# Kernel optimization log

Hardware: AMD Instinct MI355X
Metric: run time of the kernel (lower is better)

Reference implementation:

```python
import jax, jax.numpy as jnp
import numpy as np

N_E, E_DIM = 2048, 256
B, H, W = 32, 32, 32


def setup_inputs() -> dict:
    key = jax.random.key(0)
    k1, k2 = jax.random.split(key)
    z = jax.random.normal(k1, (B, E_DIM, H, W), dtype=jnp.float32)
    embedding = jax.random.normal(k2, (N_E, E_DIM), dtype=jnp.float32)
    return {"z": z, "embedding": embedding}


def reference(z, embedding):
    # z: [B, C, H, W] with C == e_dim; embedding: [n_e, e_dim]
    n_e, e_dim = embedding.shape
    b, c, h, w = z.shape
    z_nhwc = jnp.transpose(z, (0, 2, 3, 1))            # [B,H,W,C]
    z_flat = z_nhwc.reshape(-1, e_dim)                 # [L, D]
    # squared euclidean distance: ||z||^2 + ||e||^2 - 2 z.e^T
    d = (
        jnp.sum(z_flat * z_flat, axis=1, keepdims=True)
        + jnp.sum(embedding * embedding, axis=1)
        - 2.0 * jnp.einsum("ld,nd->ln", z_flat, embedding)
    )                                                  # [L, n_e]
    idx = jnp.argmin(d, axis=1)                        # [L]
    z_q = jnp.take(embedding, idx, axis=0).reshape(b, h, w, e_dim)
    # embed_ema=True -> commitment-only loss (codebook updated by EMA, not grads)
    loss = jnp.mean((jax.lax.stop_gradient(z_q) - z_nhwc) ** 2)
    # straight-through estimator
    z_q_st = z_nhwc + jax.lax.stop_gradient(z_q - z_nhwc)
    quantize = jnp.transpose(z_q_st, (0, 3, 1, 2))     # [B,C,H,W]
    # number of distinct codebook entries used (jit-safe via scatter-set)
    used = jnp.sum(jnp.zeros((n_e,), z.dtype).at[idx].set(1.0))
    index = idx.reshape(b, h, w)
    return quantize, loss, index, used
```

## Files before the change

kernel.cpp:

```cpp
#include <hip/hip_runtime.h>
#include <cfloat>

#define Dm 256
#define HW 1024
#define NE 2048
#define L_TOT 32768
#define QOFF 8388608
#define TAU 0.02f

typedef __attribute__((ext_vector_type(8))) short bf16x8;
typedef __attribute__((ext_vector_type(4))) float f32x4;
typedef const __attribute__((address_space(1))) unsigned int* as1_u32p;
typedef __attribute__((address_space(3))) unsigned int* as3_u32p;

#define GLL(gp, lp) __builtin_amdgcn_global_load_lds((as1_u32p)(gp), (as3_u32p)(lp), 16, 0, 0)

__device__ __forceinline__ unsigned short f2bf(float x) {
    unsigned u = __float_as_uint(x);
    unsigned r = (u + 0x7fffu + ((u >> 16) & 1u)) >> 16;
    return (unsigned short)r;
}
__device__ __forceinline__ float bf2f(unsigned short h) {
    return __uint_as_float(((unsigned)h) << 16);
}

__global__ void k_enorm(const float* __restrict__ emb, float* __restrict__ enorm) {
    int w = threadIdx.x >> 6, lane = threadIdx.x & 63;
    int n = blockIdx.x * 4 + w;
    const float4 v = *reinterpret_cast<const float4*>(emb + (size_t)n * Dm + lane * 4);
    double s = (double)v.x * v.x + (double)v.y * v.y + (double)v.z * v.z + (double)v.w * v.w;
    #pragma unroll
    for (int off = 32; off; off >>= 1) s += __shfl_xor(s, off);
    if (lane == 0) enorm[n] = (float)s;
}

__global__ __launch_bounds__(256) void k_split_e_norm(
    const float* __restrict__ emb, unsigned short* __restrict__ e_hi,
    unsigned short* __restrict__ e_lo, float* __restrict__ enorm)
{
    int w = threadIdx.x >> 6, lane = threadIdx.x & 63;
    int n = blockIdx.x * 4 + w;
    const float4 v = *reinterpret_cast<const float4*>(emb + (size_t)n * Dm + lane * 4);
    float vv[4] = { v.x, v.y, v.z, v.w };
    double s = (double)v.x * v.x + (double)v.y * v.y + (double)v.z * v.z + (double)v.w * v.w;
    #pragma unroll
    for (int off = 32; off; off >>= 1) s += __shfl_xor(s, off);
    if (lane == 0) enorm[n] = (float)s;
    ushort4 h4, l4;
    unsigned short* hp = (unsigned short*)&h4;
    unsigned short* lp = (unsigned short*)&l4;
    #pragma unroll
    for (int j = 0; j < 4; ++j) {
        unsigned short h = f2bf(vv[j]);
        hp[j] = h;
        lp[j] = f2bf(vv[j] - bf2f(h));
    }
    *reinterpret_cast<ushort4*>(e_hi + (size_t)n * Dm + lane * 4) = h4;
    *reinterpret_cast<ushort4*>(e_lo + (size_t)n * Dm + lane * 4) = l4;
}

__global__ __launch_bounds__(256) void k_split_z(const float* __restrict__ z,
                                                 unsigned short* __restrict__ z_hi,
                                                 unsigned short* __restrict__ z_lo,
                                                 float* __restrict__ zn_part) {
    __shared__ unsigned short zh[32][260];
    __shared__ unsigned short zl[32][260];
    __shared__ double zsum[4];
    const int b  = blockIdx.x >> 5;
    const int p0 = (blockIdx.x & 31) * 32;
    const int t  = threadIdx.x;
    const int pp = t & 31, cb = t >> 5;
    const float* zb = z + (size_t)b * (Dm * HW) + p0 + pp;
    float zs = 0.f;
    for (int ci = 0; ci < 32; ++ci) {
        int c = ci * 8 + cb;
        float x = zb[(size_t)c * HW];
        zs = fmaf(x, x, zs);
        unsigned short h = f2bf(x);
        zh[pp][c] = h;
        zl[pp][c] = f2bf(x - bf2f(h));
    }
    double d = zs;
    #pragma unroll
    for (int off = 32; off; off >>= 1) d += __shfl_xor(d, off);
    if ((t & 63) == 0) zsum[t >> 6] = d;
    __syncthreads();
    if (t == 0) zn_part[blockIdx.x] = (float)(zsum[0] + zsum[1] + zsum[2] + zsum[3]);
    const int l0 = b * 1024 + p0;
    #pragma unroll
    for (int r = 0; r < 8; ++r) {
        int id = r * 256 + t;
        int row = id >> 6, ch = id & 63;
        *reinterpret_cast<ushort4*>(z_hi + (size_t)(l0 + row) * Dm + ch * 4) =
            *reinterpret_cast<ushort4*>(&zh[row][ch * 4]);
        *reinterpret_cast<ushort4*>(z_lo + (size_t)(l0 + row) * Dm + ch * 4) =
            *reinterpret_cast<ushort4*>(&zl[row][ch * 4]);
    }
}

__global__ __launch_bounds__(512, 4) void k_score2(
    const unsigned short* __restrict__ z_hi, const unsigned short* __restrict__ z_lo,
    const unsigned short* __restrict__ e_hi, const unsigned short* __restrict__ e_lo,
    const float* __restrict__ enorm,
    float* __restrict__ pd1, float* __restrict__ pd2, int* __restrict__ pi1)
{
    __shared__ unsigned short lds[2][2][128 * 64];

    const int t    = threadIdx.x;
    const int lane = t & 63, w = t >> 6;
    const int wm = w >> 2, wn = w & 3;
    const int c15 = lane & 15, g4 = lane >> 4;

    const int bx = blockIdx.x;
    const int wg = (bx & 7) * 64 + (bx >> 3);
    const int mi = wg >> 1, ni = wg & 1;
    const int l0 = mi * 128;
    const int nbase = ni * 1024;

    auto stage = [&](int buf, const unsigned short* As, const unsigned short* Bs,
                     int nB0, int k0) {
        #pragma unroll
        for (int r = 0; r < 2; ++r) {
            int id  = r * 512 + t;
            int row = id >> 3, ch = id & 7;
            int chg = ch ^ (row & 7);
            GLL(As + (size_t)(l0 + row) * Dm + k0 + chg * 8, &lds[buf][0][id * 8]);
            GLL(Bs + (size_t)(nB0 + row) * Dm + k0 + chg * 8, &lds[buf][1][id * 8]);
        }
    };

    float d1[4][4], d2[4][4]; int i1[4][4];
    #pragma unroll
    for (int m = 0; m < 4; ++m)
        #pragma unroll
        for (int r = 0; r < 4; ++r) { d1[m][r] = 3.4e38f; d2[m][r] = 3.4e38f; i1[m][r] = 0; }

    stage(0, z_hi, e_hi, nbase, 0);
    __syncthreads();

    int cur = 0, it = 0;
    for (int nt = 0; nt < 8; ++nt) {
        f32x4 acc[4][2];
        #pragma unroll
        for (int m = 0; m < 4; ++m)
            #pragma unroll
            for (int n = 0; n < 2; ++n) acc[m][n] = (f32x4){0.f, 0.f, 0.f, 0.f};

        for (int kt = 0; kt < 12; ++kt, ++it) {
            if (it + 1 < 96) {
                int nit = it + 1;
                int nnt = nit / 12;
                int nkt = nit - nnt * 12;
                int nterm = nkt >> 2, nkc = nkt & 3;
                const unsigned short* As = (nterm == 1) ? z_lo : z_hi;
                const unsigned short* Bs = (nterm == 2) ? e_lo : e_hi;
                stage(cur ^ 1, As, Bs, nbase + nnt * 128, nkc * 64);
            }
            const unsigned short* Ab = &lds[cur][0][0];
            const unsigned short* Bb = &lds[cur][1][0];
            #pragma unroll
            for (int ks = 0; ks < 2; ++ks) {
                bf16x8 af[4], bfr[2];
                #pragma unroll
                for (int m = 0; m < 4; ++m) {
                    int row = wm * 64 + m * 16 + c15;
                    int cc  = ks * 4 + g4;
                    af[m] = *reinterpret_cast<const bf16x8*>(
                        &Ab[row * 64 + ((cc ^ (row & 7)) << 3)]);
                }
                #pragma unroll
                for (int n = 0; n < 2; ++n) {
                    int row = wn * 32 + n * 16 + c15;
                    int cc  = ks * 4 + g4;
                    bfr[n] = *reinterpret_cast<const bf16x8*>(
                        &Bb[row * 64 + ((cc ^ (row & 7)) << 3)]);
                }
                __builtin_amdgcn_s_setprio(1);
                #pragma unroll
                for (int m = 0; m < 4; ++m)
                    #pragma unroll
                    for (int n = 0; n < 2; ++n)
                        acc[m][n] = __builtin_amdgcn_mfma_f32_16x16x32_bf16(
                            af[m], bfr[n], acc[m][n], 0, 0, 0);
                __builtin_amdgcn_s_setprio(0);
            }
            __syncthreads();
            cur ^= 1;
        }
        int n0 = nbase + nt * 128;
        #pragma unroll
        for (int n = 0; n < 2; ++n) {
            int ng = n0 + wn * 32 + n * 16 + c15;
            float en = enorm[ng];
            #pragma unroll
            for (int m = 0; m < 4; ++m)
                #pragma unroll
                for (int r = 0; r < 4; ++r) {
                    float s = fmaf(-2.f, acc[m][n][r], en);
                    if (s < d1[m][r]) { d2[m][r] = d1[m][r]; d1[m][r] = s; i1[m][r] = ng; }
                    else if (s < d2[m][r]) d2[m][r] = s;
                }
        }
    }

    #pragma unroll
    for (int off = 1; off <= 8; off <<= 1) {
        #pragma unroll
        for (int m = 0; m < 4; ++m)
            #pragma unroll
            for (int r = 0; r < 4; ++r) {
                float od1 = __shfl_xor(d1[m][r], off);
                int   oi1 = __shfl_xor(i1[m][r], off);
                float od2 = __shfl_xor(d2[m][r], off);
                float nd2 = fminf(fminf(d2[m][r], od2), fmaxf(d1[m][r], od1));
                if (od1 < d1[m][r] || (od1 == d1[m][r] && oi1 < i1[m][r])) {
                    d1[m][r] = od1; i1[m][r] = oi1;
                }
                d2[m][r] = nd2;
            }
    }

    float* rs1 = (float*)&lds[0][0][0];
    float* rs2 = rs1 + 3 * 128;
    int*   ri  = (int*)(rs2 + 3 * 128);
    if (wn > 0 && c15 == 0) {
        int s = wn - 1;
        #pragma unroll
        for (int m = 0; m < 4; ++m)
            #pragma unroll
            for (int r = 0; r < 4; ++r) {
                int q = wm * 64 + m * 16 + g4 * 4 + r;
                rs1[s * 128 + q] = d1[m][r];
                rs2[s * 128 + q] = d2[m][r];
                ri [s * 128 + q] = i1[m][r];
            }
    }
    __syncthreads();
    if (wn == 0 && c15 == 0) {
        #pragma unroll
        for (int m = 0; m < 4; ++m)
            #pragma unroll
            for (int r = 0; r < 4; ++r) {
                int q = wm * 64 + m * 16 + g4 * 4 + r;
                float bd1 = d1[m][r], bd2 = d2[m][r]; int bi1 = i1[m][r];
                #pragma unroll
                for (int s = 0; s < 3; ++s) {
                    float od1 = rs1[s * 128 + q], od2 = rs2[s * 128 + q];
                    int   oi1 = ri [s * 128 + q];
                    float nd2 = fminf(fminf(bd2, od2), fmaxf(bd1, od1));
                    if (od1 < bd1 || (od1 == bd1 && oi1 < bi1)) { bd1 = od1; bi1 = oi1; }
                    bd2 = nd2;
                }
                int gq = l0 + q;
                pd1[ni * L_TOT + gq] = bd1;
                pd2[ni * L_TOT + gq] = bd2;
                pi1[ni * L_TOT + gq] = bi1;
            }
    }
}

__global__ __launch_bounds__(256) void k_merge(
    const float* __restrict__ pd1, const float* __restrict__ pd2,
    const int* __restrict__ pi1, int* __restrict__ ws_idx,
    float* __restrict__ out_idxf, float* __restrict__ used,
    int* __restrict__ flag_cnt, int* __restrict__ flag_list,
    float* __restrict__ d1_part)
{
    __shared__ float sdl[256];
    int tt = threadIdx.x;
    int gq = blockIdx.x * 256 + tt;
    float d1 = pd1[gq], d2 = pd2[gq]; int i1 = pi1[gq];
    {
        float od1 = pd1[L_TOT + gq], od2 = pd2[L_TOT + gq];
        int   oi1 = pi1[L_TOT + gq];
        float nd2 = fminf(fminf(d2, od2), fmaxf(d1, od1));
        if (od1 < d1 || (od1 == d1 && oi1 < i1)) { d1 = od1; i1 = oi1; }
        d2 = nd2;
    }
    ws_idx[gq] = i1;
    out_idxf[gq] = (float)i1;
    if (d2 - d1 < TAU) {
        int pos = atomicAdd(flag_cnt, 1);
        flag_list[pos] = gq;
    } else {
        used[i1] = 1.0f;
    }
    sdl[tt] = d1;
    __syncthreads();
    for (int st = 128; st; st >>= 1) {
        if (tt < st) sdl[tt] += sdl[tt + st];
        __syncthreads();
    }
    if (tt == 0) d1_part[blockIdx.x] = sdl[0];
}

#define BM 64
#define BN 128
#define BK 64
__global__ __launch_bounds__(256, 2) void k_argmin_f32(
    const float* __restrict__ z, const float* __restrict__ emb,
    const float* __restrict__ enorm, int* __restrict__ ws_idx,
    float* __restrict__ out_idxf, float* __restrict__ used,
    int* __restrict__ flag_cnt, int* __restrict__ flag_list)
{
    __shared__ float zl[BK][BM];
    __shared__ float el[BK][BN + 4];
    __shared__ float rd1[4][64];
    __shared__ int   ri1[4][64];
    __shared__ float rd2[4][64];

    const int t  = threadIdx.x;
    const int tq = t & 15;
    const int tn = t >> 4;
    const int l0 = blockIdx.x * BM;
    const int b  = l0 >> 10, p0 = l0 & 1023;
    const float* zb = z + (size_t)b * (Dm * HW) + p0;

    float d1[4], d2[4]; int i1[4];
    #pragma unroll
    for (int i = 0; i < 4; ++i) { d1[i] = FLT_MAX; d2[i] = FLT_MAX; i1[i] = 0; }

    for (int nt = 0; nt < NE / BN; ++nt) {
        const int n0 = nt * BN;
        float acc[4][8];
        #pragma unroll
        for (int i = 0; i < 4; ++i)
            #pragma unroll
            for (int j = 0; j < 8; ++j) acc[i][j] = 0.f;

        for (int kc = 0; kc < Dm / BK; ++kc) {
            __syncthreads();
            #pragma unroll
            for (int r = 0; r < 4; ++r) {
                int f = r * 256 + t;
                int kk = f >> 4, q4 = (f & 15) << 2;
                float4 v = *reinterpret_cast<const float4*>(zb + (size_t)(kc * BK + kk) * HW + q4);
                *reinterpret_cast<float4*>(&zl[kk][q4]) = v;
            }
            #pragma unroll
            for (int r = 0; r < 8; ++r) {
                int f = r * 256 + t;
                int n = f >> 4, k4 = (f & 15) << 2;
                float4 v = *reinterpret_cast<const float4*>(emb + (size_t)(n0 + n) * Dm + kc * BK + k4);
                el[k4 + 0][n] = v.x; el[k4 + 1][n] = v.y;
                el[k4 + 2][n] = v.z; el[k4 + 3][n] = v.w;
            }
            __syncthreads();
            #pragma unroll 4
            for (int kk = 0; kk < BK; ++kk) {
                float4 zf = *reinterpret_cast<const float4*>(&zl[kk][tq << 2]);
                float4 e0 = *reinterpret_cast<const float4*>(&el[kk][tn << 3]);
                float4 e1 = *reinterpret_cast<const float4*>(&el[kk][(tn << 3) + 4]);
                float zr[4] = { zf.x, zf.y, zf.z, zf.w };
                float er[8] = { e0.x, e0.y, e0.z, e0.w, e1.x, e1.y, e1.z, e1.w };
                #pragma unroll
                for (int i = 0; i < 4; ++i)
                    #pragma unroll
                    for (int j = 0; j < 8; ++j)
                        acc[i][j] = fmaf(zr[i], er[j], acc[i][j]);
            }
        }
        #pragma unroll
        for (int j = 0; j < 8; ++j) {
            int ng = n0 + (tn << 3) + j;
            float en = enorm[ng];
            #pragma unroll
            for (int i = 0; i < 4; ++i) {
                float s = fmaf(-2.f, acc[i][j], en);
                if (s < d1[i]) { d2[i] = d1[i]; d1[i] = s; i1[i] = ng; }
                else if (s < d2[i]) d2[i] = s;
            }
        }
    }
    #pragma unroll
    for (int off = 16; off <= 32; off <<= 1) {
        #pragma unroll
        for (int i = 0; i < 4; ++i) {
            float od1 = __shfl_xor(d1[i], off);
            int   oi1 = __shfl_xor(i1[i], off);
            float od2 = __shfl_xor(d2[i], off);
            float nd2 = fminf(fminf(d2[i], od2), fmaxf(d1[i], od1));
            bool take = (od1 < d1[i]) || (od1 == d1[i] && oi1 < i1[i]);
            if (take) { d1[i] = od1; i1[i] = oi1; }
            d2[i] = nd2;
        }
    }
    int w = t >> 6;
    if ((t & 63) < 16) {
        #pragma unroll
        for (int i = 0; i < 4; ++i) {
            rd1[w][(tq << 2) + i] = d1[i];
            ri1[w][(tq << 2) + i] = i1[i];
            rd2[w][(tq << 2) + i] = d2[i];
        }
    }
    __syncthreads();
    if (t < 64) {
        float bd1 = rd1[0][t]; int bi1 = ri1[0][t]; float bd2 = rd2[0][t];
        #pragma unroll
        for (int ww = 1; ww < 4; ++ww) {
            float od1 = rd1[ww][t]; int oi1 = ri1[ww][t]; float od2 = rd2[ww][t];
            float nd2 = fminf(fminf(bd2, od2), fmaxf(bd1, od1));
            if (od1 < bd1 || (od1 == bd1 && oi1 < bi1)) { bd1 = od1; bi1 = oi1; }
            bd2 = nd2;
        }
        int l = l0 + t;
        ws_idx[l] = bi1;
        out_idxf[l] = (float)bi1;
        if (bd2 - bd1 < TAU) {
            int pos = atomicAdd(flag_cnt, 1);
            flag_list[pos] = l;
        } else {
            used[bi1] = 1.0f;
        }
    }
}

__global__ void k_refine(const float* __restrict__ z, const float* __restrict__ emb,
                         const int* __restrict__ flag_cnt, const int* __restrict__ flag_list,
                         int* __restrict__ ws_idx, float* __restrict__ out_idxf,
                         float* __restrict__ used)
{
    __shared__ float zrow[Dm];
    __shared__ double sd[256];
    __shared__ int    si[256];
    int nf = *flag_cnt;
    for (int fi = blockIdx.x; fi < nf; fi += gridDim.x) {
        int l = flag_list[fi];
        int b = l >> 10, p = l & 1023;
        const float* zq = z + (size_t)b * (Dm * HW) + p;
        __syncthreads();
        for (int c = threadIdx.x; c < Dm; c += blockDim.x) zrow[c] = zq[(size_t)c * HW];
        __syncthreads();
        double bd = DBL_MAX; int bi = 0;
        for (int nb = 0; nb < NE / 256; ++nb) {
            int n = nb * 256 + threadIdx.x;
            const float* er = emb + (size_t)n * Dm;
            double dt0 = 0.0, dt1 = 0.0, dt2 = 0.0, dt3 = 0.0;
            double nm0 = 0.0, nm1 = 0.0, nm2 = 0.0, nm3 = 0.0;
            for (int c = 0; c < Dm; c += 4) {
                double e0 = er[c], e1 = er[c + 1], e2 = er[c + 2], e3 = er[c + 3];
                dt0 += e0 * (double)zrow[c];     nm0 += e0 * e0;
                dt1 += e1 * (double)zrow[c + 1]; nm1 += e1 * e1;
                dt2 += e2 * (double)zrow[c + 2]; nm2 += e2 * e2;
                dt3 += e3 * (double)zrow[c + 3]; nm3 += e3 * e3;
            }
            double s = (nm0 + nm1) + (nm2 + nm3) - 2.0 * ((dt0 + dt1) + (dt2 + dt3));
            if (s < bd) { bd = s; bi = n; }
        }
        sd[threadIdx.x] = bd; si[threadIdx.x] = bi;
        __syncthreads();
        for (int st = 128; st; st >>= 1) {
            if (threadIdx.x < (unsigned)st) {
                double od = sd[threadIdx.x + st]; int oi = si[threadIdx.x + st];
                if (od < sd[threadIdx.x] || (od == sd[threadIdx.x] && oi < si[threadIdx.x])) {
                    sd[threadIdx.x] = od; si[threadIdx.x] = oi;
                }
            }
            __syncthreads();
        }
        if (threadIdx.x == 0) {
            ws_idx[l] = si[0];
            out_idxf[l] = (float)si[0];
            used[si[0]] = 1.0f;
        }
        __syncthreads();
    }
}

__global__ __launch_bounds__(256) void k_gather(
    const float* __restrict__ emb, const int* __restrict__ ws_idx,
    float* __restrict__ outq)
{
    __shared__ int sidx[64];
    __shared__ float eldT[Dm][65];
    const int t = threadIdx.x;
    const int l0 = blockIdx.x * 64;
    const int b = l0 >> 10, p0 = l0 & 1023;
    if (t < 64) sidx[t] = ws_idx[l0 + t];
    __syncthreads();
    int w = t >> 6, lane = t & 63;
    for (int r = 0; r < 16; ++r) {
        int q = r * 4 + w;
        const float4 v = *reinterpret_cast<const float4*>(emb + (size_t)sidx[q] * Dm + lane * 4);
        eldT[lane * 4 + 0][q] = v.x; eldT[lane * 4 + 1][q] = v.y;
        eldT[lane * 4 + 2][q] = v.z; eldT[lane * 4 + 3][q] = v.w;
    }
    __syncthreads();
    const size_t obase = (size_t)b * (Dm * HW) + p0 + lane;
    #pragma unroll 4
    for (int it = 0; it < 64; ++it) {
        int c = w * 64 + it;
        outq[obase + (size_t)c * HW] = eldT[c][lane];
    }
}

__global__ __launch_bounds__(256) void k_gather_loss(
    const float* __restrict__ z, const float* __restrict__ emb,
    const int* __restrict__ ws_idx, float* __restrict__ outq,
    float* __restrict__ partials)
{
    __shared__ int sidx[64];
    __shared__ float eldT[Dm][65];
    __shared__ float wsum[4];
    const int t = threadIdx.x;
    const int l0 = blockIdx.x * 64;
    const int b = l0 >> 10, p0 = l0 & 1023;
    if (t < 64) sidx[t] = ws_idx[l0 + t];
    __syncthreads();
    int w = t >> 6, lane = t & 63;
    for (int r = 0; r < 16; ++r) {
        int q = r * 4 + w;
        const float4 v = *reinterpret_cast<const float4*>(emb + (size_t)sidx[q] * Dm + lane * 4);
        eldT[lane * 4 + 0][q] = v.x; eldT[lane * 4 + 1][q] = v.y;
        eldT[lane * 4 + 2][q] = v.z; eldT[lane * 4 + 3][q] = v.w;
    }
    __syncthreads();
    float ls = 0.f;
    const size_t obase = (size_t)b * (Dm * HW) + p0 + lane;
    for (int it = 0; it < 64; ++it) {
        int c = w * 64 + it;
        size_t o = obase + (size_t)c * HW;
        float qv = eldT[c][lane];
        float zv = z[o];
        outq[o] = qv;
        float df = qv - zv;
        ls = fmaf(df, df, ls);
    }
    #pragma unroll
    for (int off = 32; off; off >>= 1) ls += __shfl_xor(ls, off);
    if (lane == 0) wsum[w] = ls;
    __syncthreads();
    if (t == 0) partials[blockIdx.x] = wsum[0] + wsum[1] + wsum[2] + wsum[3];
}

__global__ void k_final(const float* __restrict__ zn_part, const float* __restrict__ d1_part,
                        const float* __restrict__ used,
                        float* __restrict__ out_loss, float* __restrict__ out_used)
{
    __shared__ double s1[256];
    __shared__ float  s2[256];
    int t = threadIdx.x;
    double a = 0.0;
    for (int i = t; i < 1024; i += 256) a += (double)zn_part[i];
    if (t < 128) a += (double)d1_part[t];
    float u = 0.f;
    for (int i = t; i < NE; i += 256) u += used[i];
    s1[t] = a; s2[t] = u;
    __syncthreads();
    for (int st = 128; st; st >>= 1) {
        if (t < st) { s1[t] += s1[t + st]; s2[t] += s2[t + st]; }
        __syncthreads();
    }
    if (t == 0) { *out_loss = (float)(s1[0] / 8388608.0); *out_used = s2[0]; }
}

__global__ void k_final_fb(const float* __restrict__ partials, const float* __restrict__ used,
                           float* __restrict__ out_loss, float* __restrict__ out_used)
{
    __shared__ float s1[256], s2[256];
    int t = threadIdx.x;
    float a = partials[t] + partials[t + 256];
    float u = 0.f;
    for (int i = t; i < NE; i += 256) u += used[i];
    s1[t] = a; s2[t] = u;
    __syncthreads();
    for (int st = 128; st; st >>= 1) {
        if (t < st) { s1[t] += s1[t + st]; s2[t] += s2[t + st]; }
        __syncthreads();
    }
    if (t == 0) { *out_loss = s1[0] / 8388608.f; *out_used = s2[0]; }
}

extern "C" void kernel_launch(void* const* d_in, const int* in_sizes, int n_in,
                              void* d_out, int out_size, void* d_ws, size_t ws_size,
                              hipStream_t stream) {
    const float* z   = (const float*)d_in[0];
    const float* emb = (const float*)d_in[1];
    float* out      = (float*)d_out;
    float* outq     = out;
    float* out_loss = out + QOFF;
    float* out_idxf = out + QOFF + 1;
    float* out_used = out + QOFF + 1 + L_TOT;

    float* ws       = (float*)d_ws;
    float* enorm    = ws;
    float* used     = ws + 2048;
    float* zn_part  = ws + 4096;
    float* d1_part  = ws + 5120;
    int*   flag_cnt = (int*)(ws + 5376);
    int*   ws_idx   = (int*)(ws + 5632);
    int*   flag_list= (int*)(ws + 5632 + L_TOT);

    unsigned short* e_hi = (unsigned short*)((char*)d_ws + 284672);
    unsigned short* e_lo = e_hi + (size_t)NE * Dm;
    unsigned short* z_hi = e_lo + (size_t)NE * Dm;
    unsigned short* z_lo = z_hi + (size_t)L_TOT * Dm;
    size_t need = 284672 + 2ull * (NE + L_TOT) * Dm * sizeof(unsigned short);

    float* pd1 = outq;
    float* pd2 = outq + 2 * L_TOT;
    int*   pi1 = (int*)(outq + 4 * L_TOT);

    hipMemsetAsync(used, 0, (size_t)3584 * 4, stream);

    if (ws_size >= need) {
        k_split_e_norm<<<NE / 4, 256, 0, stream>>>(emb, e_hi, e_lo, enorm);
        k_split_z<<<1024, 256, 0, stream>>>(z, z_hi, z_lo, zn_part);
        k_score2<<<512, 512, 0, stream>>>(z_hi, z_lo, e_hi, e_lo, enorm, pd1, pd2, pi1);
        k_merge<<<L_TOT / 256, 256, 0, stream>>>(pd1, pd2, pi1, ws_idx, out_idxf, used,
                                                 flag_cnt, flag_list, d1_part);
        k_refine<<<256, 256, 0, stream>>>(z, emb, flag_cnt, flag_list, ws_idx, out_idxf, used);
        k_gather<<<L_TOT / 64, 256, 0, stream>>>(emb, ws_idx, outq);
        k_final<<<1, 256, 0, stream>>>(zn_part, d1_part, used, out_loss, out_used);
    } else {
        k_enorm<<<NE / 4, 256, 0, stream>>>(emb, enorm);
        k_argmin_f32<<<L_TOT / BM, 256, 0, stream>>>(z, emb, enorm, ws_idx, out_idxf, used,
                                                     flag_cnt, flag_list);
        k_refine<<<256, 256, 0, stream>>>(z, emb, flag_cnt, flag_list, ws_idx, out_idxf, used);
        k_gather_loss<<<L_TOT / 64, 256, 0, stream>>>(z, emb, ws_idx, outq, zn_part);
        k_final_fb<<<1, 256, 0, stream>>>(zn_part, used, out_loss, out_used);
    }
}
```

Baseline: 248.8 us.

## Fuse split kernels, merge+gather, and drop memset in VQ pipeline

Combines the codebook and z bf16-split kernels into one launch that also zeroes the used buffer and flag counter, replacing the memset. Adds a merge+gather kernel that reduces the two partial argmin halves and immediately writes the quantized output transposed, with partials moved into the workspace so they no longer alias the output. The refine kernel now rewrites output rows for flagged points. The aim is fewer launches and less intermediate traffic, at the cost of needing a larger workspace and taking a different path when the workspace is small.

Measured after the change: 241.1 us. 1.03x faster.

```diff
diff --git a/kernel.cpp b/kernel.cpp
--- a/kernel.cpp
+++ b/kernel.cpp
@@ -34,41 +34,45 @@
     if (lane == 0) enorm[n] = (float)s;
 }
 
-__global__ __launch_bounds__(256) void k_split_e_norm(
-    const float* __restrict__ emb, unsigned short* __restrict__ e_hi,
-    unsigned short* __restrict__ e_lo, float* __restrict__ enorm)
-{
-    int w = threadIdx.x >> 6, lane = threadIdx.x & 63;
-    int n = blockIdx.x * 4 + w;
-    const float4 v = *reinterpret_cast<const float4*>(emb + (size_t)n * Dm + lane * 4);
-    float vv[4] = { v.x, v.y, v.z, v.w };
-    double s = (double)v.x * v.x + (double)v.y * v.y + (double)v.z * v.z + (double)v.w * v.w;
-    #pragma unroll
-    for (int off = 32; off; off >>= 1) s += __shfl_xor(s, off);
-    if (lane == 0) enorm[n] = (float)s;
-    ushort4 h4, l4;
-    unsigned short* hp = (unsigned short*)&h4;
-    unsigned short* lp = (unsigned short*)&l4;
-    #pragma unroll
-    for (int j = 0; j < 4; ++j) {
-        unsigned short h = f2bf(vv[j]);
-        hp[j] = h;
-        lp[j] = f2bf(vv[j] - bf2f(h));
-    }
-    *reinterpret_cast<ushort4*>(e_hi + (size_t)n * Dm + lane * 4) = h4;
-    *reinterpret_cast<ushort4*>(e_lo + (size_t)n * Dm + lane * 4) = l4;
-}
-
-__global__ __launch_bounds__(256) void k_split_z(const float* __restrict__ z,
-                                                 unsigned short* __restrict__ z_hi,
-                                                 unsigned short* __restrict__ z_lo,
-                                                 float* __restrict__ zn_part) {
+__global__ __launch_bounds__(256) void k_split(
+    const float* __restrict__ z, const float* __restrict__ emb,
+    unsigned short* __restrict__ z_hi, unsigned short* __restrict__ z_lo,
+    unsigned short* __restrict__ e_hi, unsigned short* __restrict__ e_lo,
+    float* __restrict__ enorm, float* __restrict__ zn_part,
+    float* __restrict__ used, int* __restrict__ flag_cnt)
+{
     __shared__ unsigned short zh[32][260];
     __shared__ unsigned short zl[32][260];
     __shared__ double zsum[4];
+    const int t = threadIdx.x;
+    const int w = t >> 6, lane = t & 63;
+
+    if (blockIdx.x >= 16 && blockIdx.x < 24) used[(blockIdx.x - 16) * 256 + t] = 0.f;
+    if (blockIdx.x == 24 && t == 0) *flag_cnt = 0;
+
+    if (w < 2) {
+        int n = blockIdx.x * 2 + w;
+        const float4 v = *reinterpret_cast<const float4*>(emb + (size_t)n * Dm + lane * 4);
+        float vv[4] = { v.x, v.y, v.z, v.w };
+        double s = (double)v.x * v.x + (double)v.y * v.y + (double)v.z * v.z + (double)v.w * v.w;
+        #pragma unroll
+        for (int off = 32; off; off >>= 1) s += __shfl_xor(s, off);
+        if (lane == 0) enorm[n] = (float)s;
+        ushort4 h4, l4;
+        unsigned short* hp = (unsigned short*)&h4;
+        unsigned short* lp = (unsigned short*)&l4;
+        #pragma unroll
+        for (int j = 0; j < 4; ++j) {
+            unsigned short h = f2bf(vv[j]);
+            hp[j] = h;
+            lp[j] = f2bf(vv[j] - bf2f(h));
+        }
+        *reinterpret_cast<ushort4*>(e_hi + (size_t)n * Dm + lane * 4) = h4;
+        *reinterpret_cast<ushort4*>(e_lo + (size_t)n * Dm + lane * 4) = l4;
+    }
+
     const int b  = blockIdx.x >> 5;
     const int p0 = (blockIdx.x & 31) * 32;
-    const int t  = threadIdx.x;
     const int pp = t & 31, cb = t >> 5;
     const float* zb = z + (size_t)b * (Dm * HW) + p0 + pp;
     float zs = 0.f;
@@ -83,7 +87,7 @@
     double d = zs;
     #pragma unroll
     for (int off = 32; off; off >>= 1) d += __shfl_xor(d, off);
-    if ((t & 63) == 0) zsum[t >> 6] = d;
+    if ((t & 63) == 0) zsum[w] = d;
     __syncthreads();
     if (t == 0) zn_part[blockIdx.x] = (float)(zsum[0] + zsum[1] + zsum[2] + zsum[3]);
     const int l0 = b * 1024 + p0;
@@ -259,6 +263,60 @@
     }
 }
 
+__global__ __launch_bounds__(256) void k_mg(
+    const float* __restrict__ pd1, const float* __restrict__ pd2,
+    const int* __restrict__ pi1, const float* __restrict__ emb,
+    int* __restrict__ ws_idx, float* __restrict__ out_idxf,
+    float* __restrict__ used, int* __restrict__ flag_cnt,
+    int* __restrict__ flag_list, float* __restrict__ d1_part,
+    float* __restrict__ outq)
+{
+    __shared__ int sidx[64];
+    __shared__ float eldT[Dm][65];
+    const int t = threadIdx.x;
+    const int l0 = blockIdx.x * 64;
+    const int b = l0 >> 10, p0 = l0 & 1023;
+
+    if (t < 64) {
+        int gq = l0 + t;
+        float d1 = pd1[gq], d2 = pd2[gq]; int i1 = pi1[gq];
+        float od1 = pd1[L_TOT + gq], od2 = pd2[L_TOT + gq];
+        int   oi1 = pi1[L_TOT + gq];
+        float nd2 = fminf(fminf(d2, od2), fmaxf(d1, od1));
+        if (od1 < d1 || (od1 == d1 && oi1 < i1)) { d1 = od1; i1 = oi1; }
+        d2 = nd2;
+        ws_idx[gq] = i1;
+        out_idxf[gq] = (float)i1;
+        if (d2 - d1 < TAU) {
+            int pos = atomicAdd(flag_cnt, 1);
+            flag_list[pos] = gq;
+        } else {
+            used[i1] = 1.0f;
+        }
+        sidx[t] = i1;
+        float s = d1;
+        #pragma unroll
+        for (int off = 32; off; off >>= 1) s += __shfl_xor(s, off);
+        if (t == 0) d1_part[blockIdx.x] = s;
+    }
+    __syncthreads();
+
+    int w = t >> 6, lane = t & 63;
+    for (int r = 0; r < 16; ++r) {
+        int q = r * 4 + w;
+        const float4 v = *reinterpret_cast<const float4*>(emb + (size_t)sidx[q] * Dm + lane * 4);
+        eldT[lane * 4 + 0][q] = v.x; eldT[lane * 4 + 1][q] = v.y;
+        eldT[lane * 4 + 2][q] = v.z; eldT[lane * 4 + 3][q] = v.w;
+    }
+    __syncthreads();
+    const size_t obase = (size_t)b * (Dm * HW) + p0 + lane;
+    #pragma unroll 4
+    for (int it = 0; it < 64; ++it) {
+        int c = w * 64 + it;
+        outq[obase + (size_t)c * HW] = eldT[c][lane];
+    }
+}
+
 __global__ __launch_bounds__(256) void k_merge(
     const float* __restrict__ pd1, const float* __restrict__ pd2,
     const int* __restrict__ pi1, int* __restrict__ ws_idx,
@@ -419,7 +477,7 @@
 __global__ void k_refine(const float* __restrict__ z, const float* __restrict__ emb,
                          const int* __restrict__ flag_cnt, const int* __restrict__ flag_list,
                          int* __restrict__ ws_idx, float* __restrict__ out_idxf,
-                         float* __restrict__ used)
+                         float* __restrict__ used, float* __restrict__ outq)
 {
     __shared__ float zrow[Dm];
     __shared__ double sd[256];
@@ -465,6 +523,10 @@
             used[si[0]] = 1.0f;
         }
         __syncthreads();
+        int bi0 = si[0];
+        int c = threadIdx.x;
+        outq[(size_t)b * (Dm * HW) + (size_t)c * HW + p] = emb[(size_t)bi0 * Dm + c];
+        __syncthreads();
     }
 }
 
@@ -535,7 +597,7 @@
 }
 
 __global__ void k_final(const float* __restrict__ zn_part, const float* __restrict__ d1_part,
-                        const float* __restrict__ used,
+                        int nd1, const float* __restrict__ used,
                         float* __restrict__ out_loss, float* __restrict__ out_used)
 {
     __shared__ double s1[256];
@@ -543,7 +605,7 @@
     int t = threadIdx.x;
     double a = 0.0;
     for (int i = t; i < 1024; i += 256) a += (double)zn_part[i];
-    if (t < 128) a += (double)d1_part[t];
+    for (int i = t; i < nd1; i += 256) a += (double)d1_part[i];
     float u = 0.f;
     for (int i = t; i < NE; i += 256) u += used[i];
     s1[t] = a; s2[t] = u;
@@ -588,36 +650,55 @@
     float* used     = ws + 2048;
     float* zn_part  = ws + 4096;
     float* d1_part  = ws + 5120;
-    int*   flag_cnt = (int*)(ws + 5376);
-    int*   ws_idx   = (int*)(ws + 5632);
-    int*   flag_list= (int*)(ws + 5632 + L_TOT);
-
-    unsigned short* e_hi = (unsigned short*)((char*)d_ws + 284672);
-    unsigned short* e_lo = e_hi + (size_t)NE * Dm;
-    unsigned short* z_hi = e_lo + (size_t)NE * Dm;
-    unsigned short* z_lo = z_hi + (size_t)L_TOT * Dm;
-    size_t need = 284672 + 2ull * (NE + L_TOT) * Dm * sizeof(unsigned short);
-
-    float* pd1 = outq;
-    float* pd2 = outq + 2 * L_TOT;
-    int*   pi1 = (int*)(outq + 4 * L_TOT);
-
-    hipMemsetAsync(used, 0, (size_t)3584 * 4, stream);
-
-    if (ws_size >= need) {
-        k_split_e_norm<<<NE / 4, 256, 0, stream>>>(emb, e_hi, e_lo, enorm);
-        k_split_z<<<1024, 256, 0, stream>>>(z, z_hi, z_lo, zn_part);
+    int*   flag_cnt = (int*)(ws + 5632);
+    int*   ws_idx   = (int*)(ws + 5888);
+    int*   flag_list= (int*)(ws + 5888 + L_TOT);
+
+    float* pd1w = ws + 71680;
+    float* pd2w = ws + 137216;
+    int*   pi1w = (int*)(ws + 202752);
+
+    size_t bf_bytes = 2ull * (NE + L_TOT) * Dm * sizeof(unsigned short);
+    size_t need_t1 = 268288ull * 4 + bf_bytes;
+    size_t need_t2 = 71680ull * 4 + bf_bytes;
+
+    if (ws_size >= need_t1) {
+        unsigned short* e_hi = (unsigned short*)(ws + 268288);
+        unsigned short* e_lo = e_hi + (size_t)NE * Dm;
+        unsigned short* z_hi = e_lo + (size_t)NE * Dm;
+        unsigned short* z_lo = z_hi + (size_t)L_TOT * Dm;
+        k_split<<<1024, 256, 0, stream>>>(z, emb, z_hi, z_lo, e_hi, e_lo,
+                                          enorm, zn_part, used, flag_cnt);
+        k_score2<<<512, 512, 0, stream>>>(z_hi, z_lo, e_hi, e_lo, enorm, pd1w, pd2w, pi1w);
+        k_mg<<<L_TOT / 64, 256, 0, stream>>>(pd1w, pd2w, pi1w, emb, ws_idx, out_idxf,
+                                             used, flag_cnt, flag_list, d1_part, outq);
+        k_refine<<<256, 256, 0, stream>>>(z, emb, flag_cnt, flag_list, ws_idx, out_idxf,
+                                          used, outq);
+        k_final<<<1, 256, 0, stream>>>(zn_part, d1_part, 512, used, out_loss, out_used);
+    } else if (ws_size >= need_t2) {
+        unsigned short* e_hi = (unsigned short*)(ws + 71680);
+        unsigned short* e_lo = e_hi + (size_t)NE * Dm;
+        unsigned short* z_hi = e_lo + (size_t)NE * Dm;
+        unsigned short* z_lo = z_hi + (size_t)L_TOT * Dm;
+        float* pd1 = outq;
+        float* pd2 = outq + 2 * L_TOT;
+        int*   pi1 = (int*)(outq + 4 * L_TOT);
+        k_split<<<1024, 256, 0, stream>>>(z, emb, z_hi, z_lo, e_hi, e_lo,
+                                          enorm, zn_part, used, flag_cnt);
         k_score2<<<512, 512, 0, stream>>>(z_hi, z_lo, e_hi, e_lo, enorm, pd1, pd2, pi1);
         k_merge<<<L_TOT / 256, 256, 0, stream>>>(pd1, pd2, pi1, ws_idx, out_idxf, used,
                                                  flag_cnt, flag_list, d1_part);
-        k_refine<<<256, 256, 0, stream>>>(z, emb, flag_cnt, flag_list, ws_idx, out_idxf, used);
+        k_refine<<<256, 256, 0, stream>>>(z, emb, flag_cnt, flag_list, ws_idx, out_idxf,
+                                          used, outq);
         k_gather<<<L_TOT / 64, 256, 0, stream>>>(emb, ws_idx, outq);
-        k_final<<<1, 256, 0, stream>>>(zn_part, d1_part, used, out_loss, out_used);
+        k_final<<<1, 256, 0, stream>>>(zn_part, d1_part, 128, used, out_loss, out_used);
     } else {
+        hipMemsetAsync(used, 0, (size_t)3584 * 4, stream);
         k_enorm<<<NE / 4, 256, 0, stream>>>(emb, enorm);
         k_argmin_f32<<<L_TOT / BM, 256, 0, stream>>>(z, emb, enorm, ws_idx, out_idxf, used,
                                                      flag_cnt, flag_list);
-        k_refine<<<256, 256, 0, stream>>>(z, emb, flag_cnt, flag_list, ws_idx, out_idxf, used);
+        k_refine<<<256, 256, 0, stream>>>(z, emb, flag_cnt, flag_list, ws_idx, out_idxf,
+                                          used, outq);
         k_gather_loss<<<L_TOT / 64, 256, 0, stream>>>(z, emb, ws_idx, outq, zn_part);
         k_final_fb<<<1, 256, 0, stream>>>(zn_part, used, out_loss, out_used);
     }
```
